# Optimization experiments

Measured on AMD Instinct MI355X. Metric: run time of the kernel, lower is better.

Reference implementation:

```python
import jax, jax.numpy as jnp
import numpy as np
import math

B, S, D, H = 2, 2048, 1024, 16
DK = D // H

def setup_inputs() -> dict:
    key = jax.random.key(0)
    ks = jax.random.split(key, 12)
    s = 1.0 / math.sqrt(D)
    inp = {
        'input_q': jax.random.normal(ks[0], (B, S, D), jnp.float32),
        'input_k': jax.random.normal(ks[1], (B, S, D), jnp.float32),
        'input_v': jax.random.normal(ks[2], (B, S, D), jnp.float32),
        'mask': jax.random.randint(ks[3], (B, 1, S, S), 0, 2, jnp.int32),
        'Wq': jax.random.normal(ks[4], (D, D), jnp.float32) * s,
        'bq': jnp.zeros((D,), jnp.float32),
        'Wk': jax.random.normal(ks[5], (D, D), jnp.float32) * s,
        'bk': jnp.zeros((D,), jnp.float32),
        'Wv': jax.random.normal(ks[6], (D, D), jnp.float32) * s,
        'bv': jnp.zeros((D,), jnp.float32),
        'Wo': jax.random.normal(ks[7], (D, D), jnp.float32) * s,
        'bo': jnp.zeros((D,), jnp.float32),
    }
    return inp

def reference(input_q, input_k, input_v, mask, Wq, bq, Wk, bk, Wv, bv, Wo, bo):
    # Linear projections (torch Linear: x @ W.T + b), split into heads: [B,H,S,DK]
    q = (input_q @ Wq.T + bq).reshape(B, S, H, DK).transpose(0, 2, 1, 3)
    k = (input_k @ Wk.T + bk).reshape(B, S, H, DK).transpose(0, 2, 1, 3)
    v = (input_v @ Wv.T + bv).reshape(B, S, H, DK).transpose(0, 2, 1, 3)
    scores = jnp.einsum('bhqd,bhkd->bhqk', q, k) / math.sqrt(DK)
    scores = jnp.where(mask == 0, jnp.float32(-1e9), scores)
    attn = jax.nn.softmax(scores, axis=-1)
    out = jnp.einsum('bhqk,bhkd->bhqd', attn, v)
    out = out.transpose(0, 2, 1, 3).reshape(B, S, D)
    return out @ Wo.T + bo
```

## Files before the change

### kernel.cpp

```cpp
#include <hip/hip_runtime.h>
#include <math.h>

#define kB 2
#define kS 2048
#define kD 1024
#define kH 16
#define kM (kB * kS)

#define kC 0.180336880f

typedef unsigned short u16;
typedef unsigned int u32;
typedef unsigned long long u64;
typedef short s16x8 __attribute__((ext_vector_type(8)));
typedef float f32x4 __attribute__((ext_vector_type(4)));

#if __has_builtin(__builtin_amdgcn_exp2f)
#define EXP2(x) __builtin_amdgcn_exp2f(x)
#else
#define EXP2(x) exp2f(x)
#endif

__device__ __forceinline__ u16 f2bf(float f) {
    u32 u = __float_as_uint(f);
    u += 0x7FFFu + ((u >> 16) & 1u);
    return (u16)(u >> 16);
}

__device__ __forceinline__ u32 cvt_pk_bf16(float lo, float hi) {
    u32 r;
    asm("v_cvt_pk_bf16_f32 %0, %1, %2" : "=v"(r) : "v"(lo), "v"(hi));
    return r;
}

typedef __attribute__((address_space(1))) void as1_void;
typedef __attribute__((address_space(3))) void as3_void;
__device__ __forceinline__ void async_copy16(const void* g, void* l) {
    __builtin_amdgcn_global_load_lds((as1_void*)(unsigned long long)g,
                                     (as3_void*)(unsigned)(unsigned long long)l,
                                     16, 0, 0);
}

__global__ __launch_bounds__(256) void prep(
        const float* __restrict__ xq, const float* __restrict__ xk, const float* __restrict__ xv,
        const float* __restrict__ Wq, const float* __restrict__ Wk,
        const float* __restrict__ Wv, const float* __restrict__ Wo,
        const int* __restrict__ msk,
        u16* __restrict__ xqb, u16* __restrict__ xkb, u16* __restrict__ xvb,
        u16* __restrict__ wqb, u16* __restrict__ wkb, u16* __restrict__ wvb,
        u16* __restrict__ wob, u64* __restrict__ prepM) {
    const int bid = blockIdx.x;
    const int tid = threadIdx.x;
    if (bid < 16384) {
        const float* in;
        u16* out;
        int i;
        float sc = 1.0f;
        if (bid < 12288) {
            const int z = bid >> 12;
            in = z == 0 ? xq : (z == 1 ? xk : xv);
            out = z == 0 ? xqb : (z == 1 ? xkb : xvb);
            i = (bid & 4095) * 256 + tid;
        } else {
            const int z = (bid - 12288) >> 10;
            in = z == 0 ? Wq : (z == 1 ? Wk : (z == 2 ? Wv : Wo));
            out = z == 0 ? wqb : (z == 1 ? wkb : (z == 2 ? wvb : wob));
            if (z == 0) sc = kC;
            i = ((bid - 12288) & 1023) * 256 + tid;
        }
        const float4 v = ((const float4*)in)[i];
        ushort4 o;
        o.x = f2bf(v.x * sc); o.y = f2bf(v.y * sc);
        o.z = f2bf(v.z * sc); o.w = f2bf(v.w * sc);
        ((ushort4*)out)[i] = o;
    } else {
        const int wid = (bid - 16384) * 4 + (tid >> 6);
        const int lane = tid & 63;
        const int kt = wid & 31, qb = (wid >> 5) & 127, b = wid >> 12;
        const int q = qb * 16 + (lane & 15);
        const int kbase = kt * 64 + ((lane >> 4) << 2);
        const int* mrow = msk + ((size_t)b * kS + q) * kS;
        u64 keep = 0;
#pragma unroll
        for (int c = 0; c < 4; ++c) {
            const int4 m4 = *(const int4*)(mrow + kbase + c * 16);
            const int mv[4] = {m4.x, m4.y, m4.z, m4.w};
#pragma unroll
            for (int r = 0; r < 4; ++r) {
                const u64 bl = __ballot(mv[r] != 0);
                if (lane == c * 4 + r) keep = bl;
            }
        }
        if (lane < 16)
            prepM[(((size_t)b * 128 + qb) * 32 + kt) * 16 + lane] = keep;
    }
}

template <int MODE, int TILEM>
__device__ __forceinline__ void gemm_bt_body(const u16* __restrict__ A,
                                             const u16* __restrict__ W,
                                             const float* __restrict__ bias,
                                             void* __restrict__ Cp,
                                             const float bscale) {
    constexpr int FM = TILEM / 32;
    __shared__ u16 As[TILEM * 64];
    __shared__ u16 Bs[128 * 64];
    const int tid = threadIdx.x;
    const int wave = tid >> 6, lane = tid & 63;
    const int l15 = lane & 15, quad = lane >> 4, l7 = lane & 7;
    const int wr = wave >> 1, wc = wave & 1;
    const int m0 = (MODE == 3 ? blockIdx.x : blockIdx.y) * TILEM;
    const int n0 = (MODE == 3 ? blockIdx.y : blockIdx.x) * 128;

    const int srow = lane >> 3;
    const int schk = l7 ^ srow;
    const u16* gA = A + (size_t)(m0 + (TILEM / 4) * wave + srow) * kD + schk * 8;
    const u16* gB = W + (size_t)(n0 + 32 * wave + srow) * kD + schk * 8;
    u16* lA = As + ((TILEM / 4) * wave) * 64;
    u16* lB = Bs + (32 * wave) * 64;

    f32x4 acc[FM][4];
#pragma unroll
    for (int i = 0; i < FM; ++i)
#pragma unroll
        for (int j = 0; j < 4; ++j) acc[i][j] = (f32x4)0.f;

    for (int kt = 0; kt < kD; kt += 64) {
        __syncthreads();
#pragma unroll
        for (int i = 0; i < TILEM / 32; ++i)
            async_copy16(gA + (size_t)(8 * i) * kD + kt, lA + (8 * i) * 64);
#pragma unroll
        for (int i = 0; i < 4; ++i)
            async_copy16(gB + (size_t)(8 * i) * kD + kt, lB + (8 * i) * 64);
        __syncthreads();

#pragma unroll
        for (int s = 0; s < 2; ++s) {
            const int rdoff = ((s * 4 + quad) ^ l7) * 8;
            s16x8 af[FM], bf[4];
#pragma unroll
            for (int fm = 0; fm < FM; ++fm)
                af[fm] = *(const s16x8*)(As + (wr * (TILEM / 2) + fm * 16 + l15) * 64 + rdoff);
#pragma unroll
            for (int fn = 0; fn < 4; ++fn)
                bf[fn] = *(const s16x8*)(Bs + (wc * 64 + fn * 16 + l15) * 64 + rdoff);
#pragma unroll
            for (int fm = 0; fm < FM; ++fm)
#pragma unroll
                for (int fn = 0; fn < 4; ++fn)
                    acc[fm][fn] = __builtin_amdgcn_mfma_f32_16x16x32_bf16(
                        af[fm], bf[fn], acc[fm][fn], 0, 0, 0);
        }
    }

    if constexpr (MODE == 3) {
#pragma unroll
        for (int fn = 0; fn < 4; ++fn) {
            const int sglob = n0 + wc * 64 + fn * 16 + l15;
            const int bb = sglob >> 11, ss = sglob & (kS - 1);
#pragma unroll
            for (int fm = 0; fm < FM; ++fm) {
                const int dglob = m0 + wr * (TILEM / 2) + fm * 16 + quad * 4;
                const float4 b4 = *(const float4*)(bias + dglob);
                const float bb4[4] = {b4.x * bscale, b4.y * bscale,
                                      b4.z * bscale, b4.w * bscale};
                const int hh = dglob >> 6, dd = dglob & 63;
                u16* base = (u16*)Cp + ((size_t)(bb * kH + hh) * 64 + dd) * kS + ss;
#pragma unroll
                for (int r = 0; r < 4; ++r)
                    base[(size_t)r * kS] = f2bf(acc[fm][fn][r] + bb4[r]);
            }
        }
    } else {
#pragma unroll
        for (int fn = 0; fn < 4; ++fn) {
            const int col = n0 + wc * 64 + fn * 16 + l15;
            const float bv = bias[col] * bscale;
#pragma unroll
            for (int fm = 0; fm < FM; ++fm) {
                const int row = m0 + wr * (TILEM / 2) + fm * 16 + quad * 4;
#pragma unroll
                for (int r = 0; r < 4; ++r) {
                    const float v = acc[fm][fn][r] + bv;
                    if constexpr (MODE == 0)
                        ((u16*)Cp)[(size_t)(row + r) * kD + col] = f2bf(v);
                    else
                        ((float*)Cp)[(size_t)(row + r) * kD + col] = v;
                }
            }
        }
    }
}

__global__ __launch_bounds__(256) void qkv_gemm(
        const u16* __restrict__ xq, const u16* __restrict__ xk, const u16* __restrict__ xv,
        const u16* __restrict__ wq, const u16* __restrict__ wk, const u16* __restrict__ wv,
        const float* __restrict__ bq, const float* __restrict__ bk, const float* __restrict__ bv,
        u16* __restrict__ q, u16* __restrict__ k, u16* __restrict__ vt) {
    const int z = blockIdx.z;
    if (z == 0)      gemm_bt_body<0, 128>(xq, wq, bq, q, kC);
    else if (z == 1) gemm_bt_body<0, 128>(xk, wk, bk, k, 1.f);
    else             gemm_bt_body<3, 128>(wv, xv, bv, vt, 1.f);
}

__global__ __launch_bounds__(256) void o_gemm(const u16* __restrict__ A,
                                              const u16* __restrict__ W,
                                              const float* __restrict__ bias,
                                              float* __restrict__ C) {
    gemm_bt_body<2, 64>(A, W, bias, C, 1.f);
}

__device__ __forceinline__ void attn_tile(
        const int kt, u16* __restrict__ cur, u16* __restrict__ nxt, const bool do_stage,
        const u16* __restrict__ gK0, const u16* __restrict__ gV0,
        const u64* __restrict__ mbase,
        const s16x8 bq0, const s16x8 bq1, const s16x8 onesf,
        u16* __restrict__ psrow,
        f32x4 oacc[4], f32x4& lacc,
        const int l15, const int quad, const int l7, const int wave) {
    if (do_stage) {
        async_copy16(gK0 + (size_t)(kt + 64) * kD, nxt + (8 * wave) * 64);
        async_copy16(gV0 + kt + 64, nxt + 4096 + (8 * wave) * 64);
    }
    const u64* mt = mbase + (kt >> 6) * 16;
    u64 mk[16];
#pragma unroll
    for (int i = 0; i < 16; ++i) mk[i] = mt[i];

    f32x4 s[4];
#pragma unroll
    for (int fn = 0; fn < 4; ++fn) s[fn] = (f32x4)0.f;
    __builtin_amdgcn_s_setprio(1);
#pragma unroll
    for (int kc = 0; kc < 2; ++kc) {
        const s16x8 bqf = kc ? bq1 : bq0;
#pragma unroll
        for (int fn = 0; fn < 4; ++fn) {
            const s16x8 ak = *(const s16x8*)(cur + (fn * 16 + l15) * 64 + ((kc * 4 + quad) ^ l7) * 8);
            s[fn] = __builtin_amdgcn_mfma_f32_16x16x32_bf16(ak, bqf, s[fn], 0, 0, 0);
        }
    }
    __builtin_amdgcn_s_setprio(0);

    s16x8 av[2][4];
#pragma unroll
    for (int kc = 0; kc < 2; ++kc)
#pragma unroll
        for (int fd = 0; fd < 4; ++fd)
            av[kc][fd] = *(const s16x8*)(cur + 4096 + (fd * 16 + l15) * 64 + ((kc * 4 + quad) ^ l7) * 8);

#pragma unroll
    for (int fn = 0; fn < 4; ++fn)
#pragma unroll
        for (int r = 0; r < 4; ++r) {
            const float p = EXP2(s[fn][r]);
            float pm;
            asm("v_cndmask_b32 %0, 0, %1, %2" : "=v"(pm) : "v"(p), "s"(mk[fn * 4 + r]));
            s[fn][r] = pm;
        }

#pragma unroll
    for (int fn = 0; fn < 4; ++fn) {
        uint2 o;
        o.x = cvt_pk_bf16(s[fn][0], s[fn][1]);
        o.y = cvt_pk_bf16(s[fn][2], s[fn][3]);
        const int chunk = fn * 2 + (quad >> 1);
        *(uint2*)(psrow + ((chunk ^ l7) * 8) + (quad & 1) * 4) = o;
    }

    __builtin_amdgcn_s_setprio(1);
#pragma unroll
    for (int kc = 0; kc < 2; ++kc) {
        const s16x8 bp = *(const s16x8*)(psrow + ((kc * 4 + quad) ^ l7) * 8);
        lacc = __builtin_amdgcn_mfma_f32_16x16x32_bf16(onesf, bp, lacc, 0, 0, 0);
#pragma unroll
        for (int fd = 0; fd < 4; ++fd)
            oacc[fd] = __builtin_amdgcn_mfma_f32_16x16x32_bf16(av[kc][fd], bp, oacc[fd], 0, 0, 0);
    }
    __builtin_amdgcn_s_setprio(0);
    __syncthreads();
}

__global__ __launch_bounds__(512) void attn_mfma(const u16* __restrict__ Qb,
                                                 const u16* __restrict__ Kb,
                                                 const u16* __restrict__ Vt,
                                                 const u64* __restrict__ prepM,
                                                 u16* __restrict__ Ob) {
    __shared__ u16 Bs2[2][8192];
    __shared__ u16 Ps[8192];

    const int tid = threadIdx.x;
    const int wave = tid >> 6, lane = tid & 63;
    const int l15 = lane & 15, quad = lane >> 4, l7 = lane & 7;
    const int q0 = blockIdx.x * 128;
    const int b = blockIdx.y >> 4, h = blockIdx.y & 15;

    const int srow = lane >> 3;
    const int schk = l7 ^ srow;

    {
        const u16* g0 = Qb + ((size_t)(b * kS + q0 + 16 * wave + srow)) * kD + h * 64 + schk * 8;
        async_copy16(g0, Ps + (16 * wave) * 64);
        async_copy16(g0 + 8 * kD, Ps + (16 * wave + 8) * 64);
    }
    const u16* gK0 = Kb + ((size_t)(b * kS + 8 * wave + srow)) * kD + h * 64 + schk * 8;
    const u16* gV0 = Vt + ((size_t)((b * kH + h) * 64 + 8 * wave + srow)) * kS + schk * 8;
    async_copy16(gK0, Bs2[0] + (8 * wave) * 64);
    async_copy16(gV0, Bs2[0] + 4096 + (8 * wave) * 64);

    const int wave_u = __builtin_amdgcn_readfirstlane(wave);
    const u64* mbase = prepM + (((size_t)b * 128 + blockIdx.x * 8 + wave_u) * 32) * 16;

    s16x8 onesf;
#pragma unroll
    for (int i = 0; i < 8; ++i) onesf[i] = (short)0x3F80;

    f32x4 oacc[4];
#pragma unroll
    for (int i = 0; i < 4; ++i) oacc[i] = (f32x4)0.f;
    f32x4 lacc = (f32x4)0.f;

    __syncthreads();
    s16x8 bq0, bq1;
    bq0 = *(const s16x8*)(Ps + (16 * wave + l15) * 64 + ((0 + quad) ^ l7) * 8);
    bq1 = *(const s16x8*)(Ps + (16 * wave + l15) * 64 + ((4 + quad) ^ l7) * 8);
    u16* psrow = Ps + (16 * wave + l15) * 64;

    for (int ti = 0; ti < 32; ti += 2) {
        attn_tile(ti * 64, Bs2[0], Bs2[1], true,
                  gK0, gV0, mbase, bq0, bq1, onesf, psrow, oacc, lacc,
                  l15, quad, l7, wave);
        attn_tile(ti * 64 + 64, Bs2[1], Bs2[0], ti + 2 < 32,
                  gK0, gV0, mbase, bq0, bq1, onesf, psrow, oacc, lacc,
                  l15, quad, l7, wave);
    }

    const float inv = 1.f / lacc[0];
    const size_t orow = (size_t)(b * kS + q0 + 16 * wave + l15);
#pragma unroll
    for (int fd = 0; fd < 4; ++fd) {
        uint2 o;
        o.x = cvt_pk_bf16(oacc[fd][0] * inv, oacc[fd][1] * inv);
        o.y = cvt_pk_bf16(oacc[fd][2] * inv, oacc[fd][3] * inv);
        *(uint2*)(Ob + orow * kD + h * 64 + fd * 16 + quad * 4) = o;
    }
}

extern "C" void kernel_launch(void* const* d_in, const int* in_sizes, int n_in,
                              void* d_out, int out_size, void* d_ws, size_t ws_size,
                              hipStream_t stream) {
    const float* xq = (const float*)d_in[0];
    const float* xk = (const float*)d_in[1];
    const float* xv = (const float*)d_in[2];
    const int*  msk = (const int*)d_in[3];
    const float* Wq = (const float*)d_in[4];
    const float* bq = (const float*)d_in[5];
    const float* Wk = (const float*)d_in[6];
    const float* bk = (const float*)d_in[7];
    const float* Wv = (const float*)d_in[8];
    const float* bv = (const float*)d_in[9];
    const float* Wo = (const float*)d_in[10];
    const float* bo = (const float*)d_in[11];
    float* out = (float*)d_out;

    const size_t NX = (size_t)kM * kD;
    const size_t NW = (size_t)kD * kD;

    u64* prepM = (u64*)d_ws;
    u16* p = (u16*)((char*)d_ws + (1 << 20));
    u16* xqb = p; p += NX;
    u16* xkb = p; p += NX;
    u16* xvb = p; p += NX;
    u16* wqb = p; p += NW;
    u16* wkb = p; p += NW;
    u16* wvb = p; p += NW;
    u16* wob = p; p += NW;
    u16* qb  = p; p += NX;
    u16* kb  = p; p += NX;
    u16* vtb = p; p += NX;
    u16* ab  = xqb;

    prep<<<18432, 256, 0, stream>>>(xq, xk, xv, Wq, Wk, Wv, Wo, msk,
                                    xqb, xkb, xvb, wqb, wkb, wvb, wob, prepM);

    dim3 gq(kD / 128, kM / 128, 3);
    qkv_gemm<<<gq, 256, 0, stream>>>(xqb, xkb, xvb, wqb, wkb, wvb, bq, bk, bv, qb, kb, vtb);

    dim3 ga(kS / 128, kB * kH);
    attn_mfma<<<ga, 512, 0, stream>>>(qb, kb, vtb, prepM, ab);

    dim3 go(kD / 128, kM / 64);
    o_gemm<<<go, 256, 0, stream>>>(ab, wob, bo, out);
}
```

Measured before the change: 246.6 us.

## Triple-buffer K/V tiles in attention with two-deep async prefetch

Replaces double-buffered K/V LDS staging with a three-buffer ring so loads are issued two tiles ahead. The full __syncthreads is replaced by a partial vmcnt wait plus a raw s_barrier, leaving the newest prefetch in flight across the barrier. This aims to hide global-load latency behind more MFMA work, at the cost of 16KB more LDS per block, which may reduce occupancy. It also relies on the vmcnt accounting matching the number of outstanding async copies, including the mask loads.

```diff
diff --git a/kernel.cpp b/kernel.cpp
--- a/kernel.cpp
+++ b/kernel.cpp
@@ -212,21 +212,22 @@
 }
 
 __device__ __forceinline__ void attn_tile(
-        const int kt, u16* __restrict__ cur, u16* __restrict__ nxt, const bool do_stage,
+        const int kt, u16* __restrict__ cur, u16* __restrict__ stg, const bool do_stage,
         const u16* __restrict__ gK0, const u16* __restrict__ gV0,
         const u64* __restrict__ mbase,
         const s16x8 bq0, const s16x8 bq1, const s16x8 onesf,
         u16* __restrict__ psrow,
         f32x4 oacc[4], f32x4& lacc,
         const int l15, const int quad, const int l7, const int wave) {
-    if (do_stage) {
-        async_copy16(gK0 + (size_t)(kt + 64) * kD, nxt + (8 * wave) * 64);
-        async_copy16(gV0 + kt + 64, nxt + 4096 + (8 * wave) * 64);
-    }
     const u64* mt = mbase + (kt >> 6) * 16;
     u64 mk[16];
 #pragma unroll
     for (int i = 0; i < 16; ++i) mk[i] = mt[i];
+
+    if (do_stage) {
+        async_copy16(gK0 + (size_t)(kt + 128) * kD, stg + (8 * wave) * 64);
+        async_copy16(gV0 + kt + 128, stg + 4096 + (8 * wave) * 64);
+    }
 
     f32x4 s[4];
 #pragma unroll
@@ -279,7 +280,14 @@
             oacc[fd] = __builtin_amdgcn_mfma_f32_16x16x32_bf16(av[kc][fd], bp, oacc[fd], 0, 0, 0);
     }
     __builtin_amdgcn_s_setprio(0);
-    __syncthreads();
+
+    if (do_stage)
+        asm volatile("s_waitcnt vmcnt(2)" ::: "memory");
+    else
+        asm volatile("s_waitcnt vmcnt(0)" ::: "memory");
+    __builtin_amdgcn_sched_barrier(0);
+    __builtin_amdgcn_s_barrier();
+    __builtin_amdgcn_sched_barrier(0);
 }
 
 __global__ __launch_bounds__(512) void attn_mfma(const u16* __restrict__ Qb,
@@ -287,7 +295,7 @@
                                                  const u16* __restrict__ Vt,
                                                  const u64* __restrict__ prepM,
                                                  u16* __restrict__ Ob) {
-    __shared__ u16 Bs2[2][8192];
+    __shared__ u16 Bs3[3][8192];
     __shared__ u16 Ps[8192];
 
     const int tid = threadIdx.x;
@@ -306,8 +314,10 @@
     }
     const u16* gK0 = Kb + ((size_t)(b * kS + 8 * wave + srow)) * kD + h * 64 + schk * 8;
     const u16* gV0 = Vt + ((size_t)((b * kH + h) * 64 + 8 * wave + srow)) * kS + schk * 8;
-    async_copy16(gK0, Bs2[0] + (8 * wave) * 64);
-    async_copy16(gV0, Bs2[0] + 4096 + (8 * wave) * 64);
+    async_copy16(gK0, Bs3[0] + (8 * wave) * 64);
+    async_copy16(gV0, Bs3[0] + 4096 + (8 * wave) * 64);
+    async_copy16(gK0 + (size_t)64 * kD, Bs3[1] + (8 * wave) * 64);
+    async_copy16(gV0 + 64, Bs3[1] + 4096 + (8 * wave) * 64);
 
     const int wave_u = __builtin_amdgcn_readfirstlane(wave);
     const u64* mbase = prepM + (((size_t)b * 128 + blockIdx.x * 8 + wave_u) * 32) * 16;
@@ -321,19 +331,24 @@
     for (int i = 0; i < 4; ++i) oacc[i] = (f32x4)0.f;
     f32x4 lacc = (f32x4)0.f;
 
-    __syncthreads();
+    asm volatile("s_waitcnt vmcnt(2)" ::: "memory");
+    __builtin_amdgcn_sched_barrier(0);
+    __builtin_amdgcn_s_barrier();
+    __builtin_amdgcn_sched_barrier(0);
+
     s16x8 bq0, bq1;
     bq0 = *(const s16x8*)(Ps + (16 * wave + l15) * 64 + ((0 + quad) ^ l7) * 8);
     bq1 = *(const s16x8*)(Ps + (16 * wave + l15) * 64 + ((4 + quad) ^ l7) * 8);
     u16* psrow = Ps + (16 * wave + l15) * 64;
 
-    for (int ti = 0; ti < 32; ti += 2) {
-        attn_tile(ti * 64, Bs2[0], Bs2[1], true,
+    u16* b0 = Bs3[0];
+    u16* b1 = Bs3[1];
+    u16* b2 = Bs3[2];
+    for (int ti = 0; ti < 32; ++ti) {
+        attn_tile(ti * 64, b0, b2, ti + 2 < 32,
                   gK0, gV0, mbase, bq0, bq1, onesf, psrow, oacc, lacc,
                   l15, quad, l7, wave);
-        attn_tile(ti * 64 + 64, Bs2[1], Bs2[0], ti + 2 < 32,
-                  gK0, gV0, mbase, bq0, bq1, onesf, psrow, oacc, lacc,
-                  l15, quad, l7, wave);
+        u16* t = b0; b0 = b1; b1 = b2; b2 = t;
     }
 
     const float inv = 1.f / lacc[0];
```

After: 247.6 us. Within noise of the previous version (+0.4%).

## Double-buffer GEMM LDS tiles with 32-wide k-steps and a new swizzle

Applied to the files above, without the earlier changes.

Splits the shared-memory A/B tiles into two 32-wide k buffers and prefetches the next half-tile with async copies while MFMAs run on the current one. This keeps the barrier count per 64-k step at two but overlaps global-to-LDS loads with compute. The LDS layout changes to 16-row subtiles with a rotated 4-chunk swizzle to avoid bank conflicts. The risk is lower per-stage compute depth and whether async copies actually overlap without explicit waits.

```diff
diff --git a/kernel.cpp b/kernel.cpp
--- a/kernel.cpp
+++ b/kernel.cpp
@@ -103,21 +103,19 @@
                                              void* __restrict__ Cp,
                                              const float bscale) {
     constexpr int FM = TILEM / 32;
-    __shared__ u16 As[TILEM * 64];
-    __shared__ u16 Bs[128 * 64];
+    __shared__ u16 As[2][TILEM * 32];
+    __shared__ u16 Bs[2][128 * 32];
     const int tid = threadIdx.x;
     const int wave = tid >> 6, lane = tid & 63;
-    const int l15 = lane & 15, quad = lane >> 4, l7 = lane & 7;
+    const int l15 = lane & 15, quad = lane >> 4;
     const int wr = wave >> 1, wc = wave & 1;
     const int m0 = (MODE == 3 ? blockIdx.x : blockIdx.y) * TILEM;
     const int n0 = (MODE == 3 ? blockIdx.y : blockIdx.x) * 128;
 
-    const int srow = lane >> 3;
-    const int schk = l7 ^ srow;
+    const int srow = lane >> 2;
+    const int schk = ((lane & 3) - ((lane >> 3) & 3)) & 3;
     const u16* gA = A + (size_t)(m0 + (TILEM / 4) * wave + srow) * kD + schk * 8;
     const u16* gB = W + (size_t)(n0 + 32 * wave + srow) * kD + schk * 8;
-    u16* lA = As + ((TILEM / 4) * wave) * 64;
-    u16* lB = Bs + (32 * wave) * 64;
 
     f32x4 acc[FM][4];
 #pragma unroll
@@ -125,33 +123,43 @@
 #pragma unroll
         for (int j = 0; j < 4; ++j) acc[i][j] = (f32x4)0.f;
 
+    auto STAGE = [&](int kt, u16* dA, u16* dB) {
+#pragma unroll
+        for (int i = 0; i < TILEM / 64; ++i)
+            async_copy16(gA + (size_t)(16 * i) * kD + kt,
+                         dA + (wave * (TILEM / 64) + i) * 512);
+#pragma unroll
+        for (int i = 0; i < 2; ++i)
+            async_copy16(gB + (size_t)(16 * i) * kD + kt,
+                         dB + (wave * 2 + i) * 512);
+    };
+
+    const int ro = ((quad + (l15 >> 1)) & 3) * 8;
+    auto COMPUTE = [&](const u16* sA, const u16* sB) {
+        s16x8 af[FM], bf[4];
+#pragma unroll
+        for (int fm = 0; fm < FM; ++fm)
+            af[fm] = *(const s16x8*)(sA + (wr * (TILEM / 32) + fm) * 512 + l15 * 32 + ro);
+#pragma unroll
+        for (int fn = 0; fn < 4; ++fn)
+            bf[fn] = *(const s16x8*)(sB + (wc * 4 + fn) * 512 + l15 * 32 + ro);
+#pragma unroll
+        for (int fm = 0; fm < FM; ++fm)
+#pragma unroll
+            for (int fn = 0; fn < 4; ++fn)
+                acc[fm][fn] = __builtin_amdgcn_mfma_f32_16x16x32_bf16(
+                    af[fm], bf[fn], acc[fm][fn], 0, 0, 0);
+    };
+
+    STAGE(0, As[0], Bs[0]);
+    __syncthreads();
     for (int kt = 0; kt < kD; kt += 64) {
+        if (kt + 32 < kD) STAGE(kt + 32, As[1], Bs[1]);
+        COMPUTE(As[0], Bs[0]);
         __syncthreads();
-#pragma unroll
-        for (int i = 0; i < TILEM / 32; ++i)
-            async_copy16(gA + (size_t)(8 * i) * kD + kt, lA + (8 * i) * 64);
-#pragma unroll
-        for (int i = 0; i < 4; ++i)
-            async_copy16(gB + (size_t)(8 * i) * kD + kt, lB + (8 * i) * 64);
+        if (kt + 64 < kD) STAGE(kt + 64, As[0], Bs[0]);
+        COMPUTE(As[1], Bs[1]);
         __syncthreads();
-
-#pragma unroll
-        for (int s = 0; s < 2; ++s) {
-            const int rdoff = ((s * 4 + quad) ^ l7) * 8;
-            s16x8 af[FM], bf[4];
-#pragma unroll
-            for (int fm = 0; fm < FM; ++fm)
-                af[fm] = *(const s16x8*)(As + (wr * (TILEM / 2) + fm * 16 + l15) * 64 + rdoff);
-#pragma unroll
-            for (int fn = 0; fn < 4; ++fn)
-                bf[fn] = *(const s16x8*)(Bs + (wc * 64 + fn * 16 + l15) * 64 + rdoff);
-#pragma unroll
-            for (int fm = 0; fm < FM; ++fm)
-#pragma unroll
-                for (int fn = 0; fn < 4; ++fn)
-                    acc[fm][fn] = __builtin_amdgcn_mfma_f32_16x16x32_bf16(
-                        af[fm], bf[fn], acc[fm][fn], 0, 0, 0);
-        }
     }
 
     if constexpr (MODE == 3) {
```

Result: no change. 249.1 us (+1.0%).
